# Kernel tuning notes

Measured on AMD Instinct MI355X. Metric: run time of the kernel, lower is better.

The kernel has to match this reference:

```python
import jax, jax.numpy as jnp
import numpy as np

D_MODEL = 1024
NHEAD = 16
D_HEAD = D_MODEL // NHEAD


def setup_inputs() -> dict:
    key = jax.random.key(0)
    ks = jax.random.split(key, 5)
    s_in = 1.0 / np.sqrt(D_MODEL)
    x = jax.random.normal(ks[0], (2, 2048, D_MODEL), dtype=jnp.float32)
    Wqkv = jax.random.uniform(ks[1], (D_MODEL, 3 * D_MODEL), jnp.float32, -s_in, s_in)
    bqkv = jax.random.uniform(ks[2], (3 * D_MODEL,), jnp.float32, -s_in, s_in)
    Wproj = jax.random.uniform(ks[3], (D_MODEL, D_MODEL), jnp.float32, -s_in, s_in)
    bproj = jax.random.uniform(ks[4], (D_MODEL,), jnp.float32, -s_in, s_in)
    return {"x": x, "Wqkv": Wqkv, "bqkv": bqkv, "Wproj": Wproj, "bproj": bproj}


def reference(x, Wqkv, bqkv, Wproj, bproj):
    B, N, D = x.shape
    qkv = x @ Wqkv + bqkv                       # [B, N, 3D]
    q, k, v = jnp.split(qkv, 3, axis=-1)
    # [B, N, D] -> [B, H, N, d]
    def to_heads(t):
        return t.reshape(B, N, NHEAD, D_HEAD).transpose(0, 2, 1, 3)
    q, k, v = to_heads(q), to_heads(k), to_heads(v)
    scale = 1.0 / np.sqrt(D_HEAD).astype(np.float32)
    attn = jnp.einsum('bhqd,bhkd->bhqk', q, k) * scale
    attn = jax.nn.softmax(attn, axis=-1)
    y = jnp.einsum('bhqk,bhkd->bhqd', attn, v)  # [B, H, N, d]
    y = y.transpose(0, 2, 1, 3).reshape(B, N, D)
    return y @ Wproj + bproj
```

## Files before the change

kernel.cpp:

```cpp
#include <hip/hip_runtime.h>
#include <hip/hip_bf16.h>
#include <stdint.h>

typedef __hip_bfloat16 bf16;
typedef __attribute__((ext_vector_type(8))) short short8;
typedef __attribute__((ext_vector_type(4))) float f32x4;

#define QSCALE 0.18033688011f

__device__ __forceinline__ float fast_exp2(float x) {
#if __has_builtin(__builtin_amdgcn_exp2f)
  return __builtin_amdgcn_exp2f(x);
#else
  return exp2f(x);
#endif
}

__device__ __forceinline__ uint32_t pack2_bf16(float a, float b) {
#if __has_builtin(__builtin_amdgcn_cvt_pk_bf16_f32)
  typedef __attribute__((ext_vector_type(2))) __bf16 bf16x2;
  bf16x2 v = __builtin_amdgcn_cvt_pk_bf16_f32(a, b);
  return __builtin_bit_cast(uint32_t, v);
#else
  uint32_t ua = __builtin_bit_cast(uint32_t, a);
  uint32_t ub = __builtin_bit_cast(uint32_t, b);
  ua += 0x7FFF + ((ua >> 16) & 1);
  ub += 0x7FFF + ((ub >> 16) & 1);
  return (ua >> 16) | (ub & 0xFFFF0000u);
#endif
}

__device__ __forceinline__ void gload_lds16(const bf16* g, bf16* l) {
#if __has_builtin(__builtin_amdgcn_global_load_lds)
  __builtin_amdgcn_global_load_lds(
      (const __attribute__((address_space(1))) void*)(uintptr_t)g,
      (__attribute__((address_space(3))) void*)(uint32_t)(uintptr_t)l,
      16, 0, 0);
#else
  int lane = threadIdx.x & 63;
  *(short8*)(l + lane * 8) = *(const short8*)(g + lane * 8);
#endif
}

#define DMA_BARRIER() \
  asm volatile("s_waitcnt vmcnt(0) lgkmcnt(0)\n\ts_barrier" ::: "memory")

__device__ __forceinline__ void transpose_tile(const float* __restrict__ in,
                                               bf16* __restrict__ out,
                                               int R, int C, int bx, int by,
                                               bf16 (*t)[72]) {
  const int r0 = by * 64, c0 = bx * 64;
  const int rr = threadIdx.x >> 3, cc = (threadIdx.x & 7) * 8;
#pragma unroll
  for (int rep = 0; rep < 2; ++rep) {
    int y = rr + rep * 32;
    const float* p = in + (size_t)(r0 + y) * C + c0 + cc;
    f32x4 v0 = *(const f32x4*)p;
    f32x4 v1 = *(const f32x4*)(p + 4);
#pragma unroll
    for (int j = 0; j < 4; ++j) {
      t[cc + j][y] = __float2bfloat16(v0[j]);
      t[cc + 4 + j][y] = __float2bfloat16(v1[j]);
    }
  }
  __syncthreads();
#pragma unroll
  for (int rep = 0; rep < 2; ++rep) {
    int y = rr + rep * 32;
    short8 v = *(const short8*)&t[y][cc];
    *(short8*)(out + (size_t)(c0 + y) * R + r0 + cc) = v;
  }
}

__global__ __launch_bounds__(256)
void prep_k(const float* __restrict__ x, bf16* __restrict__ xb,
            const float* __restrict__ Wqkv, bf16* __restrict__ WtQkv,
            const float* __restrict__ Wproj, bf16* __restrict__ WtP) {
  __shared__ __align__(16) bf16 t[64][72];
  const int bid = blockIdx.x;
  if (bid < 2048) {
    int i = (bid * 256 + threadIdx.x) * 8;
    f32x4 v0 = *(const f32x4*)(x + i);
    f32x4 v1 = *(const f32x4*)(x + i + 4);
    short8 r;
    bf16* rb = (bf16*)&r;
#pragma unroll
    for (int j = 0; j < 4; ++j) {
      rb[j] = __float2bfloat16(v0[j]);
      rb[4 + j] = __float2bfloat16(v1[j]);
    }
    *(short8*)(xb + i) = r;
  } else if (bid < 2048 + 768) {
    int b = bid - 2048;
    transpose_tile(Wqkv, WtQkv, 1024, 3072, b % 48, b / 48, t);
  } else {
    int b = bid - 2816;
    transpose_tile(Wproj, WtP, 1024, 1024, b % 16, b / 16, t);
  }
}

template <int MODE, int TM>
__global__ __launch_bounds__(256, (TM == 128) ? 3 : 2)
void gemm_bt(const bf16* __restrict__ A, const bf16* __restrict__ Bt,
             const float* __restrict__ bias, float* __restrict__ outp,
             bf16* __restrict__ Qd, bf16* __restrict__ Kd, bf16* __restrict__ Vt,
             int M, int Nn, int K) {
  constexpr int MI = TM / 32;
  constexpr int BUFE = TM * 32 + 4096;
  __shared__ __align__(16) bf16 smem[2 * BUFE];

  const int tid = threadIdx.x;
  const int wave = tid >> 6, lane = tid & 63;
  const int quad = lane >> 4, l16 = lane & 15;
  const int mw = (wave >> 1) * (TM / 2), nw = (wave & 1) * 64;

  const int nwg = gridDim.x * gridDim.y;
  const int ord = blockIdx.y * gridDim.x + blockIdx.x;
  const int wg = (ord & 7) * (nwg >> 3) + (ord >> 3);
  const int m_blk = (wg / gridDim.x) * TM, n_blk = (wg % gridDim.x) * 128;

  f32x4 acc[MI][4];
#pragma unroll
  for (int i = 0; i < MI; ++i)
#pragma unroll
    for (int j = 0; j < 4; ++j) acc[i][j] = (f32x4){0.f, 0.f, 0.f, 0.f};

  const int rowA = lane >> 2, colA = (lane & 3) * 8;
  const int chunkB = wave * 2;
  const bf16* gB = Bt + (size_t)(n_blk + chunkB * 16 + rowA) * K + colA;
  const int chunkA = (TM == 128) ? wave * 2 : wave;
  const bf16* gA = A + (size_t)(m_blk + chunkA * 16 + rowA) * K + colA;

  const int oA0 = chunkA * 512;
  const int oA1 = (chunkA + 1) * 512;
  const int oB0 = TM * 32 + chunkB * 512;
  const int oB1 = TM * 32 + (chunkB + 1) * 512;

  gload_lds16(gA, smem + oA0);
  if (TM == 128) gload_lds16(gA + 16 * K, smem + oA1);
  gload_lds16(gB, smem + oB0);
  gload_lds16(gB + 16 * K, smem + oB1);
  DMA_BARRIER();

  for (int kt = 0; kt < K; kt += 32) {
    const int cur = (kt >> 5) & 1;
    bf16* bufc = smem + cur * BUFE;

    if (kt + 32 < K) {
      bf16* bufn = smem + (cur ^ 1) * BUFE;
      gload_lds16(gA + kt + 32, bufn + oA0);
      if (TM == 128) gload_lds16(gA + 16 * K + kt + 32, bufn + oA1);
      gload_lds16(gB + kt + 32, bufn + oB0);
      gload_lds16(gB + 16 * K + kt + 32, bufn + oB1);
    }

    short8 af[MI], bfv[4];
#pragma unroll
    for (int i = 0; i < MI; ++i)
      af[i] = *(const short8*)&bufc[(mw + i * 16 + l16) * 32 + quad * 8];
#pragma unroll
    for (int j = 0; j < 4; ++j)
      bfv[j] = *(const short8*)&bufc[TM * 32 + (nw + j * 16 + l16) * 32 + quad * 8];
#pragma unroll
    for (int i = 0; i < MI; ++i)
#pragma unroll
      for (int j = 0; j < 4; ++j)
        acc[i][j] = __builtin_amdgcn_mfma_f32_16x16x32_bf16(af[i], bfv[j],
                                                            acc[i][j], 0, 0, 0);

    DMA_BARRIER();
  }

  if (MODE == 0) {
    float bval[4];
#pragma unroll
    for (int j = 0; j < 4; ++j) bval[j] = bias[n_blk + nw + j * 16 + l16];

    const int part = n_blk >> 10;
    const int b = m_blk >> 11;
    const int tloc = m_blk & 2047;
    const int h0 = (n_blk & 1023) >> 6;

#pragma unroll
    for (int p = 0; p < 2; ++p) {
      __syncthreads();
      if ((nw >> 6) == p) {
        if (part == 2) {
#pragma unroll
          for (int i = 0; i < MI; ++i)
#pragma unroll
            for (int j = 0; j < 4; ++j) {
              const int dh = j * 16 + l16;
              const int t0 = mw + i * 16 + quad * 4;
              uint2 pk;
              pk.x = pack2_bf16(acc[i][j][0] + bval[j], acc[i][j][1] + bval[j]);
              pk.y = pack2_bf16(acc[i][j][2] + bval[j], acc[i][j][3] + bval[j]);
              *(uint2*)&smem[dh * 136 + t0] = pk;
            }
        } else {
          const float sc = (part == 0) ? QSCALE : 1.0f;
#pragma unroll
          for (int i = 0; i < MI; ++i)
#pragma unroll
            for (int j = 0; j < 4; ++j) {
              const int d = j * 16 + l16;
              const int t0 = mw + i * 16 + quad * 4;
#pragma unroll
              for (int r = 0; r < 4; ++r)
                smem[(t0 + r) * 72 + d] =
                    __float2bfloat16((acc[i][j][r] + bval[j]) * sc);
            }
        }
      }
      __syncthreads();
      const size_t bh = (size_t)(b * 16 + h0 + p);
      if (part == 2) {
#pragma unroll
        for (int it = 0; it < 4; ++it) {
          const int dl = (tid >> 4) + it * 16;
          const int t8 = (tid & 15) * 8;
          const int t8s = (t8 & 64) | ((t8 ^ ((dl & 7) << 3)) & 63);
          short8 v = *(const short8*)&smem[dl * 136 + t8];
          *(short8*)&Vt[(bh * 64 + dl) * 2048 + tloc + t8s] = v;
        }
      } else {
        bf16* dst = (part == 0) ? Qd : Kd;
#pragma unroll
        for (int it = 0; it < 4; ++it) {
          const int row = (tid >> 3) + it * 32;
          const int col8 = (tid & 7) * 8;
          const int c8 = (part == 1) ? (col8 ^ ((row & 7) << 3)) : col8;
          short8 v = *(const short8*)&smem[row * 72 + col8];
          *(short8*)&dst[(bh * 2048 + tloc + row) * 64 + c8] = v;
        }
      }
    }
  } else {
#pragma unroll
    for (int j = 0; j < 4; ++j) {
      const int ncol = n_blk + nw + j * 16 + l16;
      const float bval = bias[ncol];
#pragma unroll
      for (int i = 0; i < MI; ++i) {
        const int mrow0 = m_blk + mw + i * 16 + quad * 4;
#pragma unroll
        for (int r = 0; r < 4; ++r)
          outp[(size_t)(mrow0 + r) * Nn + ncol] = acc[i][j][r] + bval;
      }
    }
  }
}

__global__ __launch_bounds__(256, 4)
void attn_kernel(const bf16* __restrict__ Qg, const bf16* __restrict__ Kg,
                 const bf16* __restrict__ Vt, bf16* __restrict__ yg) {
  __shared__ __align__(16) char pool[32768];
  bf16* KsB = (bf16*)pool;
  bf16* VtsB = (bf16*)(pool + 16384);

  const int tid = threadIdx.x;
  const int wave = tid >> 6, lane = tid & 63;
  const int quad = lane >> 4, l16 = lane & 15;
  const int qh = wave & 1, kvh = wave >> 1;

  const int bx0 = blockIdx.x;
  const int bx = ((bx0 & 7) << 7) | (bx0 >> 3);
  const int qt = bx & 31;
  const int bh = bx >> 5;

  const bf16* Qb = Qg + ((size_t)bh * 2048 + qt * 64) * 64;
  const bf16* Kb = Kg + (size_t)bh * 2048 * 64;
  const bf16* Vtb = Vt + (size_t)bh * 64 * 2048;

  short8 qf[2][2];
#pragma unroll
  for (int qblk = 0; qblk < 2; ++qblk)
#pragma unroll
    for (int ks = 0; ks < 2; ++ks)
      qf[qblk][ks] = *(const short8*)(
          Qb + (size_t)(qh * 32 + qblk * 16 + l16) * 64 + ks * 32 + quad * 8);

  const int sj = wave * 2;
  const bf16* kg = Kb + sj * 512 + lane * 8;
  const bf16* vg = Vtb + (size_t)(sj * 8 + (lane >> 3)) * 2048 +
                   (lane & 7) * 8;

  int kfo[2][2];
#pragma unroll
  for (int kvblk = 0; kvblk < 2; ++kvblk)
#pragma unroll
    for (int ks = 0; ks < 2; ++ks)
      kfo[kvblk][ks] = (kvh * 32 + kvblk * 16 + l16) * 64 +
                       (((ks * 4 + quad) ^ (l16 & 7)) << 3);
  int vbo[4][2];
#pragma unroll
  for (int dblk = 0; dblk < 4; ++dblk) {
    const int d = dblk * 16 + l16;
#pragma unroll
    for (int kvblk = 0; kvblk < 2; ++kvblk) {
      const int ct = kvh * 4 + kvblk * 2 + (quad >> 1);
      vbo[dblk][kvblk] = d * 64 + ((ct ^ (d & 7)) << 3) + (quad & 1) * 4;
    }
  }

#pragma unroll
  for (int j = 0; j < 2; ++j) {
    gload_lds16(kg + j * 512, KsB + sj * 512 + j * 512);
    gload_lds16(vg + (size_t)j * 16384, VtsB + sj * 512 + j * 512);
  }
  DMA_BARRIER();

  f32x4 yacc[2][4];
#pragma unroll
  for (int qblk = 0; qblk < 2; ++qblk)
#pragma unroll
    for (int dblk = 0; dblk < 4; ++dblk)
      yacc[qblk][dblk] = (f32x4){0.f, 0.f, 0.f, 0.f};
  f32x4 sum_acc[2];
  sum_acc[0] = (f32x4){0.f, 0.f, 0.f, 0.f};
  sum_acc[1] = (f32x4){0.f, 0.f, 0.f, 0.f};

  uint4 ones_u;
  ones_u.x = ones_u.y = ones_u.z = ones_u.w = 0x3F803F80u;
  const short8 ones8 = __builtin_bit_cast(short8, ones_u);

  for (int kt = 0; kt < 2048; kt += 64) {
    const int cur = (kt >> 6) & 1;

    if (kt + 64 < 2048) {
      bf16* Kdst = KsB + (cur ^ 1) * 4096;
      bf16* Vdst = VtsB + (cur ^ 1) * 4096;
#pragma unroll
      for (int j = 0; j < 2; ++j) {
        gload_lds16(kg + (kt + 64) * 64 + j * 512, Kdst + sj * 512 + j * 512);
        gload_lds16(vg + kt + 64 + (size_t)j * 16384, Vdst + sj * 512 + j * 512);
      }
    }
    const bf16* KsC = KsB + cur * 4096;
    const bf16* VtsC = VtsB + cur * 4096;

    short8 kf[2][2];
#pragma unroll
    for (int kvblk = 0; kvblk < 2; ++kvblk)
#pragma unroll
      for (int ks = 0; ks < 2; ++ks)
        kf[kvblk][ks] = *(const short8*)(KsC + kfo[kvblk][ks]);

    short8 pa8[2];
#pragma unroll
    for (int qblk = 0; qblk < 2; ++qblk) {
      f32x4 s0 = (f32x4){0.f, 0.f, 0.f, 0.f};
      f32x4 s1 = (f32x4){0.f, 0.f, 0.f, 0.f};
      s0 = __builtin_amdgcn_mfma_f32_16x16x32_bf16(kf[0][0], qf[qblk][0], s0, 0, 0, 0);
      s0 = __builtin_amdgcn_mfma_f32_16x16x32_bf16(kf[0][1], qf[qblk][1], s0, 0, 0, 0);
      s1 = __builtin_amdgcn_mfma_f32_16x16x32_bf16(kf[1][0], qf[qblk][0], s1, 0, 0, 0);
      s1 = __builtin_amdgcn_mfma_f32_16x16x32_bf16(kf[1][1], qf[qblk][1], s1, 0, 0, 0);
      float p0 = fast_exp2(s0[0]), p1 = fast_exp2(s0[1]);
      float p2 = fast_exp2(s0[2]), p3 = fast_exp2(s0[3]);
      float p4 = fast_exp2(s1[0]), p5 = fast_exp2(s1[1]);
      float p6 = fast_exp2(s1[2]), p7 = fast_exp2(s1[3]);
      uint4 u;
      u.x = pack2_bf16(p0, p1);
      u.y = pack2_bf16(p2, p3);
      u.z = pack2_bf16(p4, p5);
      u.w = pack2_bf16(p6, p7);
      pa8[qblk] = __builtin_bit_cast(short8, u);
      sum_acc[qblk] = __builtin_amdgcn_mfma_f32_16x16x32_bf16(
          pa8[qblk], ones8, sum_acc[qblk], 0, 0, 0);
    }

#pragma unroll
    for (int dblk = 0; dblk < 4; ++dblk) {
      uint2 lo = *(const uint2*)(VtsC + vbo[dblk][0]);
      uint2 hi = *(const uint2*)(VtsC + vbo[dblk][1]);
      uint4 u;
      u.x = lo.x; u.y = lo.y; u.z = hi.x; u.w = hi.y;
      short8 vb8 = __builtin_bit_cast(short8, u);
      yacc[0][dblk] = __builtin_amdgcn_mfma_f32_16x16x32_bf16(
          pa8[0], vb8, yacc[0][dblk], 0, 0, 0);
      yacc[1][dblk] = __builtin_amdgcn_mfma_f32_16x16x32_bf16(
          pa8[1], vb8, yacc[1][dblk], 0, 0, 0);
    }

    DMA_BARRIER();
  }

  __syncthreads();
  float* red = (float*)pool;
  float* sred = (float*)(pool + 16384);
  if (kvh == 1) {
#pragma unroll
    for (int qblk = 0; qblk < 2; ++qblk) {
#pragma unroll
      for (int dblk = 0; dblk < 4; ++dblk) {
        const int f = (qh * 2 + qblk) * 4 + dblk;
        *(f32x4*)&red[(f * 64 + quad * 16 + l16) * 4] = yacc[qblk][dblk];
      }
      if (l16 == 0)
        *(f32x4*)&sred[(qh * 2 + qblk) * 16 + quad * 4] = sum_acc[qblk];
    }
  }
  __syncthreads();
  if (kvh == 0) {
    const int b = bh >> 4, h = bh & 15;
    const size_t rowbase = (size_t)b * 2048 + qt * 64;
#pragma unroll
    for (int qblk = 0; qblk < 2; ++qblk) {
      f32x4 sp = *(const f32x4*)&sred[(qh * 2 + qblk) * 16 + quad * 4];
#pragma unroll
      for (int dblk = 0; dblk < 4; ++dblk) {
        const int f = (qh * 2 + qblk) * 4 + dblk;
        f32x4 o = *(const f32x4*)&red[(f * 64 + quad * 16 + l16) * 4];
#pragma unroll
        for (int r = 0; r < 4; ++r) yacc[qblk][dblk][r] += o[r];
      }
#pragma unroll
      for (int r = 0; r < 4; ++r) {
        const float inv = 1.f / (sum_acc[qblk][r] + sp[r]);
        const int rr = qh * 32 + qblk * 16 + quad * 4 + r;
#pragma unroll
        for (int dblk = 0; dblk < 4; ++dblk)
          yg[(rowbase + rr) * 1024 + h * 64 + dblk * 16 + l16] =
              __float2bfloat16(yacc[qblk][dblk][r] * inv);
      }
    }
  }
}

extern "C" void kernel_launch(void* const* d_in, const int* in_sizes, int n_in,
                              void* d_out, int out_size, void* d_ws, size_t ws_size,
                              hipStream_t stream) {
  const float* x = (const float*)d_in[0];
  const float* Wqkv = (const float*)d_in[1];
  const float* bqkv = (const float*)d_in[2];
  const float* Wproj = (const float*)d_in[3];
  const float* bproj = (const float*)d_in[4];
  float* out = (float*)d_out;

  if (ws_size < (size_t)40 * 1024 * 1024) return;

  char* ws = (char*)d_ws;
  bf16* xb    = (bf16*)(ws + 0);
  bf16* yd    = (bf16*)(ws + 0);
  bf16* WtQkv = (bf16*)(ws + 8388608);
  bf16* WtP   = (bf16*)(ws + 14680064);
  bf16* Qd    = (bf16*)(ws + 16777216);
  bf16* Kd    = (bf16*)(ws + 25165824);
  bf16* Vten  = (bf16*)(ws + 33554432);

  prep_k<<<3072, 256, 0, stream>>>(x, xb, Wqkv, WtQkv, Wproj, WtP);
  gemm_bt<0, 128><<<dim3(24, 32), 256, 0, stream>>>(
      xb, WtQkv, bqkv, nullptr, Qd, Kd, Vten, 4096, 3072, 1024);
  attn_kernel<<<dim3(1024), 256, 0, stream>>>(Qd, Kd, Vten, yd);
  gemm_bt<1, 64><<<dim3(8, 64), 256, 0, stream>>>(
      yd, WtP, bproj, out, nullptr, nullptr, nullptr, 4096, 1024, 1024);
}
```

Baseline: 187.1 us.

## Use partial vmcnt waits so prefetch loads overlap compute in GEMM and attention loops

Replaces the full vmcnt(0) wait at the end of each K-loop iteration with a partial vmcnt(N) wait placed after issuing the next tile's async global-to-LDS loads. Only the current buffer's loads must finish before compute, so the next tile's loads stay in flight during the MFMAs. The last iteration issues a redundant reload of the final tile, which keeps the outstanding-load count uniform. The end-of-iteration barrier now waits only on LDS reads, which removes the write-after-read hazard on the double buffer. Correctness relies on the vmcnt values matching the number of loads issued per wave.

```diff
diff --git a/kernel.cpp b/kernel.cpp
--- a/kernel.cpp
+++ b/kernel.cpp
@@ -42,6 +42,12 @@
 #endif
 }
 
+#define VM4_BARRIER() \
+  asm volatile("s_waitcnt vmcnt(4)\n\ts_barrier" ::: "memory")
+#define VM3_BARRIER() \
+  asm volatile("s_waitcnt vmcnt(3)\n\ts_barrier" ::: "memory")
+#define LDSR_BARRIER() \
+  asm volatile("s_waitcnt lgkmcnt(0)\n\ts_barrier" ::: "memory")
 #define DMA_BARRIER() \
   asm volatile("s_waitcnt vmcnt(0) lgkmcnt(0)\n\ts_barrier" ::: "memory")
 
@@ -140,19 +146,21 @@
   if (TM == 128) gload_lds16(gA + 16 * K, smem + oA1);
   gload_lds16(gB, smem + oB0);
   gload_lds16(gB + 16 * K, smem + oB1);
-  DMA_BARRIER();
 
   for (int kt = 0; kt < K; kt += 32) {
     const int cur = (kt >> 5) & 1;
     bf16* bufc = smem + cur * BUFE;
 
-    if (kt + 32 < K) {
+    {
+      const int kn = (kt + 32 < K) ? (kt + 32) : (K - 32);
       bf16* bufn = smem + (cur ^ 1) * BUFE;
-      gload_lds16(gA + kt + 32, bufn + oA0);
-      if (TM == 128) gload_lds16(gA + 16 * K + kt + 32, bufn + oA1);
-      gload_lds16(gB + kt + 32, bufn + oB0);
-      gload_lds16(gB + 16 * K + kt + 32, bufn + oB1);
-    }
+      gload_lds16(gA + kn, bufn + oA0);
+      if (TM == 128) gload_lds16(gA + 16 * K + kn, bufn + oA1);
+      gload_lds16(gB + kn, bufn + oB0);
+      gload_lds16(gB + 16 * K + kn, bufn + oB1);
+    }
+
+    if constexpr (TM == 128) VM4_BARRIER(); else VM3_BARRIER();
 
     short8 af[MI], bfv[4];
 #pragma unroll
@@ -168,8 +176,10 @@
         acc[i][j] = __builtin_amdgcn_mfma_f32_16x16x32_bf16(af[i], bfv[j],
                                                             acc[i][j], 0, 0, 0);
 
-    DMA_BARRIER();
-  }
+    LDSR_BARRIER();
+  }
+
+  DMA_BARRIER();
 
   if (MODE == 0) {
     float bval[4];
@@ -308,7 +318,6 @@
     gload_lds16(kg + j * 512, KsB + sj * 512 + j * 512);
     gload_lds16(vg + (size_t)j * 16384, VtsB + sj * 512 + j * 512);
   }
-  DMA_BARRIER();
 
   f32x4 yacc[2][4];
 #pragma unroll
@@ -327,15 +336,19 @@
   for (int kt = 0; kt < 2048; kt += 64) {
     const int cur = (kt >> 6) & 1;
 
-    if (kt + 64 < 2048) {
+    {
+      const int kn = (kt + 64 < 2048) ? (kt + 64) : (2048 - 64);
       bf16* Kdst = KsB + (cur ^ 1) * 4096;
       bf16* Vdst = VtsB + (cur ^ 1) * 4096;
 #pragma unroll
       for (int j = 0; j < 2; ++j) {
-        gload_lds16(kg + (kt + 64) * 64 + j * 512, Kdst + sj * 512 + j * 512);
-        gload_lds16(vg + kt + 64 + (size_t)j * 16384, Vdst + sj * 512 + j * 512);
-      }
-    }
+        gload_lds16(kg + kn * 64 + j * 512, Kdst + sj * 512 + j * 512);
+        gload_lds16(vg + kn + (size_t)j * 16384, Vdst + sj * 512 + j * 512);
+      }
+    }
+
+    VM4_BARRIER();
+
     const bf16* KsC = KsB + cur * 4096;
     const bf16* VtsC = VtsB + cur * 4096;
 
@@ -382,10 +395,10 @@
           pa8[1], vb8, yacc[1][dblk], 0, 0, 0);
     }
 
-    DMA_BARRIER();
-  }
-
-  __syncthreads();
+    LDSR_BARRIER();
+  }
+
+  DMA_BARRIER();
   float* red = (float*)pool;
   float* sred = (float*)(pool + 16384);
   if (kvh == 1) {
```

New measurement: 185.6 us. Within noise of the previous version (-0.8%).
